# Kernel tuning notes

Measured on AMD Instinct MI355X. Metric: run time of the kernel, lower is better.

## Reference

```python
import jax, jax.numpy as jnp
import numpy as np
import math

B, L, D_MODEL = 2, 2048, 1024
N_HEADS, D_HEAD = 16, 64
ROPE_BASE = 10000.0
PERIODS = (24, 168)
LAMBDAS = (0.5, 0.25)
NEG_INF = jnp.float32(-jnp.inf)


def _alibi_slopes(n_heads):
    # n_heads is a power of two here (16), so only the simple branch is needed
    start = 2.0 ** (-2.0 ** (-(math.log2(n_heads) - 3)))
    return jnp.asarray([start * (start ** i) for i in range(n_heads)], dtype=jnp.float32)


def _apply_rope(x, cos_t, sin_t):
    # x: [B,H,L,Dh]; cos_t/sin_t: [1,1,L,Dh//2]
    x1, x2 = x[..., 0::2], x[..., 1::2]
    xr1 = x1 * cos_t - x2 * sin_t
    xr2 = x1 * sin_t + x2 * cos_t
    return jnp.stack([xr1, xr2], axis=-1).reshape(x.shape)


def setup_inputs() -> dict:
    key = jax.random.key(0)
    ks = jax.random.split(key, 5)
    d = D_MODEL
    return {
        "x": jax.random.normal(ks[0], (B, L, d), dtype=jnp.float32),
        "Wq": jax.random.normal(ks[1], (d, d), dtype=jnp.float32) * 0.02,
        "bq": jnp.zeros((d,), dtype=jnp.float32),
        "Wk": jax.random.normal(ks[2], (d, d), dtype=jnp.float32) * 0.02,
        "bk": jnp.zeros((d,), dtype=jnp.float32),
        "Wv": jax.random.normal(ks[3], (d, d), dtype=jnp.float32) * 0.02,
        "bv": jnp.zeros((d,), dtype=jnp.float32),
        "Wo": jax.random.normal(ks[4], (d, d), dtype=jnp.float32) * 0.02,
        "bo": jnp.zeros((d,), dtype=jnp.float32),
    }


def reference(x, Wq, bq, Wk, bk, Wv, bv, Wo, bo):
    Bn, Ln, Dn = x.shape
    H, Dh = N_HEADS, D_HEAD

    def proj(W, b):
        return (x @ W + b).reshape(Bn, Ln, H, Dh).transpose(0, 2, 1, 3)  # [B,H,L,Dh]

    q, k, v = proj(Wq, bq), proj(Wk, bk), proj(Wv, bv)

    # RoPE angles: theta[l, m] = l / base^(2m/Dh)
    inv = 1.0 / (ROPE_BASE ** (jnp.arange(0, Dh, 2, dtype=jnp.float32) / Dh))
    theta = jnp.arange(Ln, dtype=jnp.float32)[:, None] * inv[None, :]  # [L, Dh/2]
    cos_t = jnp.cos(theta)[None, None]
    sin_t = jnp.sin(theta)[None, None]
    q = _apply_rope(q, cos_t, sin_t)
    k = _apply_rope(k, cos_t, sin_t)

    scale = 1.0 / math.sqrt(Dh)
    attn = jnp.einsum("bhid,bhjd->bhij", q, k) * scale  # [B,H,L,L]

    i = jnp.arange(Ln)[:, None]
    j = jnp.arange(Ln)[None, :]

    # ALiBi bias: -slope * relu(j - i), per head
    slopes = _alibi_slopes(H)  # [H]
    dist = (j - i).astype(jnp.float32)
    attn = attn + (-slopes[None, :, None, None]) * jax.nn.relu(dist)[None, None]

    # periodic cosine bias
    d_abs = jnp.abs(dist)
    pb = jnp.zeros_like(d_abs)
    for P, lam in zip(PERIODS, LAMBDAS):
        pb = pb + lam * jnp.cos(2.0 * math.pi * d_abs / float(P))
    attn = attn + pb[None, None]

    # causal mask (torch: attn + full(-inf).triu(1))
    attn = jnp.where((j > i)[None, None], NEG_INF, attn)

    p = jax.nn.softmax(attn, axis=-1)  # dropout=0 -> identity
    out = jnp.einsum("bhij,bhjd->bhid", p, v)
    out = out.transpose(0, 2, 1, 3).reshape(Bn, Ln, Dn)
    return out @ Wo + bo, p
```

## Files before the change

### kernel.cpp

```cpp
#include <hip/hip_runtime.h>
#include <math.h>

#define B_  2
#define L_  2048
#define D_  1024
#define H_  16
#define DH_ 64
#define BL_ (B_*L_)

typedef unsigned short u16;
typedef __attribute__((ext_vector_type(8))) short short8;
typedef __attribute__((ext_vector_type(4))) float f32x4;
typedef __attribute__((ext_vector_type(4))) unsigned short u16x4;

template<bool V> struct BC { static constexpr bool value = V; };

#define WS_XB   0
#define WS_WT4  2097152
#define WS_QB   4194304
#define WS_KB   6291456
#define WS_VT   8388608
#define WS_AOB  10485760
#define WS_COS  12582912
#define WS_SIN  12648448
#define WS_PBL  12713984

__device__ __forceinline__ u16 f2b(float f) {
  union { float f; unsigned u; } v; v.f = f;
  unsigned r = (v.u + 0x7fffu + ((v.u >> 16) & 1u)) >> 16;
  return (u16)r;
}
__device__ __forceinline__ u16x4 f2b4(float a, float b, float c, float d) {
  u16x4 u; u.x = f2b(a); u.y = f2b(b); u.z = f2b(c); u.w = f2b(d); return u;
}
__device__ __forceinline__ float bf2f(u16 u) {
  union { unsigned u; float f; } v; v.u = ((unsigned)u) << 16; return v.f;
}
__device__ __forceinline__ void gl_lds16(const void* g, void* l) {
  __builtin_amdgcn_global_load_lds(
      (const __attribute__((address_space(1))) unsigned int*)g,
      (__attribute__((address_space(3))) unsigned int*)l, 16, 0, 0);
}
__device__ __forceinline__ void nt_store4(float x, float y, float z, float w, float* p) {
  f32x4 v = (f32x4){x, y, z, w};
  __builtin_nontemporal_store(v, (f32x4*)p);
}

__global__ void fill_tables(float* __restrict__ costab, float* __restrict__ sintab,
                            float* __restrict__ pbl) {
  int idx = blockIdx.x * 256 + threadIdx.x;
  if (idx < L_ * 32) {
    int l = idx >> 5, tp = idx & 31;
    double inv = pow(10000.0, -2.0 * (double)tp / 64.0);
    double th  = (double)l * inv;
    costab[idx] = (float)cos(th);
    sintab[idx] = (float)sin(th);
  }
  if (idx < L_) {
    double d = (double)idx;
    double v = 0.5  * cos(6.283185307179586 * d / 24.0)
             + 0.25 * cos(6.283185307179586 * d / 168.0);
    pbl[idx] = (float)(v * 1.4426950408889634);
  }
}

__global__ __launch_bounds__(256) void xcast(const float* __restrict__ x, u16* __restrict__ xb) {
  const size_t i = ((size_t)blockIdx.x * 256 + threadIdx.x) * 8;
  float4 a = *(const float4*)(x + i);
  float4 b = *(const float4*)(x + i + 4);
  u16 us[8] = { f2b(a.x),f2b(a.y),f2b(a.z),f2b(a.w), f2b(b.x),f2b(b.y),f2b(b.z),f2b(b.w) };
  *(short8*)(xb + i) = *(short8*)us;
}

__global__ __launch_bounds__(256) void wtrans4(const float* __restrict__ W0, const float* __restrict__ W1,
                                               const float* __restrict__ W2, const float* __restrict__ W3,
                                               u16* __restrict__ Wt) {
  __shared__ u16 tt[64][80];
  const int z = blockIdx.z;
  const float* W = (z == 0) ? W0 : (z == 1) ? W1 : (z == 2) ? W2 : W3;
  u16* Wtz = Wt + (size_t)z * 1024 * 1024;
  const int k0 = blockIdx.x << 6, n0 = blockIdx.y << 6;
  const int t = threadIdx.x;
  {
    const int r = t >> 4, c4 = (t & 15) << 2;
    for (int rr = r; rr < 64; rr += 16) {
      float4 v = *(const float4*)(W + (size_t)(k0 + rr) * D_ + n0 + c4);
      tt[c4+0][rr] = f2b(v.x); tt[c4+1][rr] = f2b(v.y);
      tt[c4+2][rr] = f2b(v.z); tt[c4+3][rr] = f2b(v.w);
    }
  }
  __syncthreads();
  const int n = t >> 2, kc = (t & 3) << 4;
  u16* dst = Wtz + (size_t)(n0 + n) * D_ + k0 + kc;
  #pragma unroll
  for (int u = 0; u < 16; ++u) dst[u] = tt[n][kc + u];
}

template<int KIND>
__global__ __launch_bounds__(256) void gemm_k(
    const u16* __restrict__ Ag, const u16* __restrict__ Bg,
    const float* __restrict__ b0, const float* __restrict__ b1, const float* __restrict__ b2,
    const float* __restrict__ costab, const float* __restrict__ sintab,
    u16* __restrict__ O0, u16* __restrict__ O1, u16* __restrict__ O2,
    float* __restrict__ Cout)
{
  __shared__ u16 As[8192];
  __shared__ u16 Bs[8192];
  const int t = threadIdx.x, w = t >> 6, lane = t & 63;
  const int lt = lane & 15, lg = lane >> 4;
  const int row0 = blockIdx.x << 7;
  const int gy   = blockIdx.y;
  const int col0 = gy << 7;
  const int wm = (w & 1) << 6, wn = (w >> 1) << 6;
  const int proj = (KIND == 1) ? (gy >> 3) : 0;
  const bool swp = (KIND == 0) || (proj < 2);

  const int srow = lane >> 3;
  const int gch  = (lane & 7) ^ (srow & 7);
  const u16* aptr[4]; const u16* bptr[4];
  char* adst[4]; char* bdst[4];
  #pragma unroll
  for (int u = 0; u < 4; ++u) {
    const int rl = w * 32 + u * 8 + srow;
    aptr[u] = Ag + (size_t)(row0 + rl) * 1024 + gch * 8;
    bptr[u] = Bg + (size_t)(col0 + rl) * 1024 + gch * 8;
    adst[u] = (char*)As + (w * 32 + u * 8) * 128;
    bdst[u] = (char*)Bs + (w * 32 + u * 8) * 128;
  }
  int aoff[2][4], boff[2][4];
  #pragma unroll
  for (int ks = 0; ks < 2; ++ks)
    #pragma unroll
    for (int q = 0; q < 4; ++q) {
      const int ra = wm + q * 16 + lt;
      aoff[ks][q] = ra * 128 + (((ks * 4 + lg) ^ (ra & 7)) << 4);
      const int rb = wn + q * 16 + lt;
      boff[ks][q] = rb * 128 + (((ks * 4 + lg) ^ (rb & 7)) << 4);
    }

  f32x4 acc[4][4];
  #pragma unroll
  for (int i = 0; i < 4; ++i)
    #pragma unroll
    for (int j = 0; j < 4; ++j) acc[i][j] = (f32x4){0.f,0.f,0.f,0.f};

  auto loop = [&](auto SW) {
    for (int kt = 0; kt < 16; ++kt) {
      #pragma unroll
      for (int u = 0; u < 4; ++u) {
        gl_lds16(aptr[u] + kt * 64, adst[u]);
        gl_lds16(bptr[u] + kt * 64, bdst[u]);
      }
      __syncthreads();
      #pragma unroll
      for (int ks = 0; ks < 2; ++ks) {
        short8 af[4], bf[4];
        #pragma unroll
        for (int q = 0; q < 4; ++q) {
          af[q] = *(const short8*)((const char*)As + aoff[ks][q]);
          bf[q] = *(const short8*)((const char*)Bs + boff[ks][q]);
        }
        #pragma unroll
        for (int mi = 0; mi < 4; ++mi)
          #pragma unroll
          for (int nj = 0; nj < 4; ++nj) {
            if constexpr (decltype(SW)::value)
              acc[mi][nj] = __builtin_amdgcn_mfma_f32_16x16x32_bf16(bf[nj], af[mi], acc[mi][nj], 0, 0, 0);
            else
              acc[mi][nj] = __builtin_amdgcn_mfma_f32_16x16x32_bf16(af[mi], bf[nj], acc[mi][nj], 0, 0, 0);
          }
      }
      __syncthreads();
    }
  };
  if (swp) loop(BC<true>{}); else loop(BC<false>{});

  if constexpr (KIND == 0) {
    #pragma unroll
    for (int mi = 0; mi < 4; ++mi) {
      const int m = row0 + wm + mi * 16 + lt;
      #pragma unroll
      for (int nj = 0; nj < 4; ++nj) {
        const int nb = col0 + wn + nj * 16 + (lg << 2);
        float4 bb = *(const float4*)(b0 + nb);
        nt_store4(acc[mi][nj][0] + bb.x, acc[mi][nj][1] + bb.y,
                  acc[mi][nj][2] + bb.z, acc[mi][nj][3] + bb.w,
                  Cout + (size_t)m * 1024 + nb);
      }
    }
  } else if (proj < 2) {
    const float* bias = proj ? b1 : b0;
    u16* Ob = proj ? O1 : O0;
    const int col0p = (gy & 7) << 7;
    #pragma unroll
    for (int mi = 0; mi < 4; ++mi) {
      const int m = row0 + wm + mi * 16 + lt;
      const int bb_ = m >> 11, lpos = m & (L_ - 1);
      #pragma unroll
      for (int nj = 0; nj < 4; ++nj) {
        const int nb = col0p + wn + nj * 16 + (lg << 2);
        const int d0 = nb & 63, h = nb >> 6;
        float4 ba = *(const float4*)(bias + nb);
        const float o0 = acc[mi][nj][0] + ba.x, o1 = acc[mi][nj][1] + ba.y;
        const float o2 = acc[mi][nj][2] + ba.z, o3 = acc[mi][nj][3] + ba.w;
        const float* ct = costab + lpos * 32 + (d0 >> 1);
        const float* st = sintab + lpos * 32 + (d0 >> 1);
        const float c0 = ct[0], c1 = ct[1], s0 = st[0], s1 = st[1];
        const float r0 = o0 * c0 - o1 * s0, r1 = o0 * s0 + o1 * c0;
        const float r2 = o2 * c1 - o3 * s1, r3 = o2 * s1 + o3 * c1;
        *(u16x4*)(Ob + ((size_t)(bb_ * 16 + h) * L_ + lpos) * 64 + d0) = f2b4(r0, r1, r2, r3);
      }
    }
  } else {
    const int col0p = (gy & 7) << 7;
    #pragma unroll
    for (int mi = 0; mi < 4; ++mi) {
      const int lb = row0 + wm + mi * 16 + (lg << 2);
      const int bb_ = lb >> 11;
      #pragma unroll
      for (int nj = 0; nj < 4; ++nj) {
        const int n = col0p + wn + nj * 16 + lt;
        const int h = n >> 6, dh = n & 63;
        const float bv1 = b2[n];
        *(u16x4*)(O2 + ((size_t)(bb_ * 16 + h) * 64 + dh) * L_ + (lb & (L_ - 1))) =
            f2b4(acc[mi][nj][0] + bv1, acc[mi][nj][1] + bv1,
                 acc[mi][nj][2] + bv1, acc[mi][nj][3] + bv1);
      }
    }
  }
}

__global__ __launch_bounds__(512, 4) void attn_mfma(
    const u16* __restrict__ Qb, const u16* __restrict__ Kb, const u16* __restrict__ Vt,
    const float* __restrict__ pbg, float* __restrict__ Pout, u16* __restrict__ AOb)
{
  __shared__ u16 PL[33 * 16 * 64];
  __shared__ float PVacc[2][16][64];
  __shared__ float lsbuf[8][2][16];
  const int t = threadIdx.x, w = t >> 6, lane = t & 63;
  const int lt = lane & 15, lg = lane >> 4;
  const int wg = blockIdx.x + (blockIdx.y << 6);
  const int sid = (wg & 7) * 256 + (wg >> 3);
  const int bh = sid >> 6, pr = sid & 63;
  const int b = bh >> 4, h = bh & 15;
  const int sA = pr, sB = 127 - pr;
  const int kvA = (sA >> 2) + 1, kvB = (sB >> 2) + 1;
  const int swz = (lt & 7) << 4;
  const float C1 = 0.18033688011112042f;
  char* PLb = (char*)PL;

  f32x4 oaccA[4], oaccB[4];
  #pragma unroll
  for (int dt = 0; dt < 4; ++dt) {
    oaccA[dt] = (f32x4){0.f,0.f,0.f,0.f};
    oaccB[dt] = (f32x4){0.f,0.f,0.f,0.f};
  }
  float lsumA = 0.f, lsumB = 0.f;

  auto tile = [&](int s, int kvt, const short8& q0, const short8& q1,
                  f32x4* oacc, float& lsum, int pb0, int rstride, bool masked) {
    const int j0 = kvt << 6;
    const int i  = s * 16 + lt;
    const u16* kp = Kb + ((size_t)bh * L_ + j0 + lt) * 64 + lg * 8;
    short8 kf[8];
    #pragma unroll
    for (int jt = 0; jt < 4; ++jt) {
      kf[2*jt]   = *(const short8*)(kp + jt * 1024);
      kf[2*jt+1] = *(const short8*)(kp + jt * 1024 + 32);
    }
    f32x4 z[4];
    #pragma unroll
    for (int jt = 0; jt < 4; ++jt) {
      f32x4 zz = (f32x4){0.f,0.f,0.f,0.f};
      zz = __builtin_amdgcn_mfma_f32_16x16x32_bf16(kf[2*jt],   q0, zz, 0, 0, 0);
      zz = __builtin_amdgcn_mfma_f32_16x16x32_bf16(kf[2*jt+1], q1, zz, 0, 0, 0);
      z[jt] = zz;
    }
    const u16* vp = Vt + ((size_t)bh * 64 + lt) * L_ + j0 + lg * 8;
    short8 vf[8];
    #pragma unroll
    for (int dt = 0; dt < 4; ++dt) {
      vf[2*dt]   = *(const short8*)(vp + dt * 16 * L_);
      vf[2*dt+1] = *(const short8*)(vp + dt * 16 * L_ + 32);
    }
    #pragma unroll
    for (int jt = 0; jt < 4; ++jt) {
      const int jb = j0 + jt * 16 + (lg << 2);
      const int dd = i - jb;
      float pr4[4];
      if (masked) {
        #pragma unroll
        for (int r = 0; r < 4; ++r) {
          const int d  = dd - r;
          const int dc = d < 0 ? 0 : d;
          const float pe = exp2f(fmaf(z[jt][r], C1, pbg[dc]));
          pr4[r] = d < 0 ? 0.f : pe;
          lsum += pr4[r];
        }
      } else {
        #pragma unroll
        for (int r = 0; r < 4; ++r) {
          pr4[r] = exp2f(fmaf(z[jt][r], C1, pbg[dd - r]));
          lsum += pr4[r];
        }
      }
      *(u16x4*)(PLb + pb0 + lt * rstride + ((kvt * 128 + jt * 32 + lg * 8) ^ swz)) =
          f2b4(pr4[0], pr4[1], pr4[2], pr4[3]);
    }
    short8 pa0 = *(const short8*)(PLb + pb0 + lt * rstride + ((kvt * 128 + lg * 16) ^ swz));
    short8 pa1 = *(const short8*)(PLb + pb0 + lt * rstride + ((kvt * 128 + 64 + lg * 16) ^ swz));
    #pragma unroll
    for (int dt = 0; dt < 4; ++dt) {
      oacc[dt] = __builtin_amdgcn_mfma_f32_16x16x32_bf16(pa0, vf[2*dt],   oacc[dt], 0, 0, 0);
      oacc[dt] = __builtin_amdgcn_mfma_f32_16x16x32_bf16(pa1, vf[2*dt+1], oacc[dt], 0, 0, 0);
    }
  };

  {
    const u16* qpA = Qb + ((size_t)bh * L_ + sA * 16 + lt) * 64 + lg * 8;
    const short8 qA0 = *(const short8*)(qpA), qA1 = *(const short8*)(qpA + 32);
    for (int kvt = w; kvt < kvA; kvt += 8)
      tile(sA, kvt, qA0, qA1, oaccA, lsumA, 0, kvA << 7, kvt == kvA - 1);
  }
  {
    const u16* qpB = Qb + ((size_t)bh * L_ + sB * 16 + lt) * 64 + lg * 8;
    const short8 qB0 = *(const short8*)(qpB), qB1 = *(const short8*)(qpB + 32);
    const int st0 = (8 + w - (kvA & 7)) & 7;
    for (int kvt = st0; kvt < kvB; kvt += 8)
      tile(sB, kvt, qB0, qB1, oaccB, lsumB, kvA << 11, kvB << 7, kvt == kvB - 1);
  }

  lsumA += __shfl_xor(lsumA, 16); lsumA += __shfl_xor(lsumA, 32);
  lsumB += __shfl_xor(lsumB, 16); lsumB += __shfl_xor(lsumB, 32);
  if (lane < 16) { lsbuf[w][0][lt] = lsumA; lsbuf[w][1][lt] = lsumB; }
  __syncthreads();

  {
    const int rowslot = t >> 4, ct = t & 15;
    const int st = rowslot >> 4, rl = rowslot & 15;
    const int s_ = st ? sB : sA;
    const int i  = s_ * 16 + rl;
    float den = 0.f;
    #pragma unroll
    for (int ww = 0; ww < 8; ++ww) den += lsbuf[ww][st][rl];
    const float rv = 1.f / den;
    const char* rb = PLb + (st ? (kvA << 11) : 0) + rl * ((st ? kvB : kvA) << 7);
    const int rsw = (rl & 7) << 4;
    float* prow = Pout + ((size_t)bh * L_ + i) * L_;
    const int lim4 = i >> 2;
    for (int cc = 0; cc < 8; ++cc) {
      const int c4b = ct + cc * 64;
      u16x4 dv[4];
      #pragma unroll
      for (int u = 0; u < 4; ++u) {
        const int c4 = c4b + u * 16;
        dv[u] = (c4 <= lim4) ? *(const u16x4*)(rb + ((c4 << 3) ^ rsw))
                             : (u16x4){0, 0, 0, 0};
      }
      #pragma unroll
      for (int u = 0; u < 4; ++u) {
        const int c4 = c4b + u * 16;
        float ox = 0.f, oy = 0.f, oz = 0.f, ow = 0.f;
        if (c4 <= lim4) {
          ox = bf2f(dv[u].x) * rv; oy = bf2f(dv[u].y) * rv;
          oz = bf2f(dv[u].z) * rv; ow = bf2f(dv[u].w) * rv;
          if (c4 == lim4) {
            const int j0c = c4 << 2;
            if (j0c + 1 > i) oy = 0.f;
            if (j0c + 2 > i) oz = 0.f;
            if (j0c + 3 > i) ow = 0.f;
          }
        }
        nt_store4(ox, oy, oz, ow, prow + (c4 << 2));
      }
    }
  }

  for (int rr = 0; rr < 8; ++rr) {
    if (w == rr) {
      #pragma unroll
      for (int dt = 0; dt < 4; ++dt)
        #pragma unroll
        for (int r = 0; r < 4; ++r) {
          if (rr == 0) {
            PVacc[0][(lg << 2) + r][dt * 16 + lt] = oaccA[dt][r];
            PVacc[1][(lg << 2) + r][dt * 16 + lt] = oaccB[dt][r];
          } else {
            PVacc[0][(lg << 2) + r][dt * 16 + lt] += oaccA[dt][r];
            PVacc[1][(lg << 2) + r][dt * 16 + lt] += oaccB[dt][r];
          }
        }
    }
    __syncthreads();
  }

  {
    const int st = t >> 8, rl = (t >> 4) & 15, c0 = (t & 15) << 2;
    float den = 0.f;
    #pragma unroll
    for (int ww = 0; ww < 8; ++ww) den += lsbuf[ww][st][rl];
    const float rv = 1.f / den;
    const int s_ = st ? sB : sA;
    const int i = s_ * 16 + rl;
    u16x4 o = f2b4(PVacc[st][rl][c0] * rv, PVacc[st][rl][c0 + 1] * rv,
                   PVacc[st][rl][c0 + 2] * rv, PVacc[st][rl][c0 + 3] * rv);
    *(u16x4*)(AOb + ((size_t)(b * L_ + i)) * 1024 + h * 64 + c0) = o;
  }
}

extern "C" void kernel_launch(void* const* d_in, const int* in_sizes, int n_in,
                              void* d_out, int out_size, void* d_ws, size_t ws_size,
                              hipStream_t stream) {
  const float* x  = (const float*)d_in[0];
  const float* Wq = (const float*)d_in[1];
  const float* bq = (const float*)d_in[2];
  const float* Wk = (const float*)d_in[3];
  const float* bk = (const float*)d_in[4];
  const float* Wv = (const float*)d_in[5];
  const float* bv = (const float*)d_in[6];
  const float* Wo = (const float*)d_in[7];
  const float* bo = (const float*)d_in[8];

  float* out  = (float*)d_out;
  float* Pout = out + (size_t)BL_ * D_;

  float* ws = (float*)d_ws;
  u16* XB  = (u16*)(ws + WS_XB);
  u16* WT4 = (u16*)(ws + WS_WT4);
  u16* QB  = (u16*)(ws + WS_QB);
  u16* KB  = (u16*)(ws + WS_KB);
  u16* VT  = (u16*)(ws + WS_VT);
  u16* AOB = (u16*)(ws + WS_AOB);
  float* cosT = ws + WS_COS;
  float* sinT = ws + WS_SIN;
  float* pblG = ws + WS_PBL;

  fill_tables<<<256, 256, 0, stream>>>(cosT, sinT, pblG);
  xcast<<<2048, 256, 0, stream>>>(x, XB);
  wtrans4<<<dim3(16,16,4), 256, 0, stream>>>(Wq, Wk, Wv, Wo, WT4);

  gemm_k<1><<<dim3(32,24), 256, 0, stream>>>(XB, WT4, bq, bk, bv, cosT, sinT,
                                             QB, KB, VT, nullptr);

  attn_mfma<<<dim3(64,32), 512, 0, stream>>>(QB, KB, VT, pblG, Pout, AOB);

  gemm_k<0><<<dim3(32,8), 256, 0, stream>>>(AOB, WT4 + (size_t)3*1024*1024, bo,
                                            nullptr, nullptr, nullptr, nullptr,
                                            nullptr, nullptr, nullptr, out);
}
```

Baseline: 285.9 us.

## Stage periodic bias in LDS, remap GEMM blocks, store P rows per wavefront

Three separate changes. The GEMM kernels remap block indices so that consecutive workgroups are spread across XCD-strided groups, aiming for better L2 locality. The attention kernel copies the periodic-bias table into the PVacc shared buffer before the main loop, so the per-element bias lookups read LDS instead of global memory; this costs an extra barrier and reuses PVacc. The probability writeback now gives each wavefront whole rows, so every store instruction covers a contiguous 1 KB span of a row rather than several rows.

```diff
diff --git a/kernel.cpp b/kernel.cpp
--- a/kernel.cpp
+++ b/kernel.cpp
@@ -108,8 +108,12 @@
   __shared__ u16 Bs[8192];
   const int t = threadIdx.x, w = t >> 6, lane = t & 63;
   const int lt = lane & 15, lg = lane >> 4;
-  const int row0 = blockIdx.x << 7;
-  const int gy   = blockIdx.y;
+  const int wg = blockIdx.x + (blockIdx.y << 5);
+  int sid;
+  if constexpr (KIND == 1) sid = (wg & 7) * 96 + (wg >> 3);
+  else                     sid = (wg & 7) * 32 + (wg >> 3);
+  const int row0 = (sid & 31) << 7;
+  const int gy   = sid >> 5;
   const int col0 = gy << 7;
   const int wm = (w & 1) << 6, wn = (w >> 1) << 6;
   const int proj = (KIND == 1) ? (gy >> 3) : 0;
@@ -237,8 +241,10 @@
   __shared__ u16 PL[33 * 16 * 64];
   __shared__ float PVacc[2][16][64];
   __shared__ float lsbuf[8][2][16];
+  float* pbl = &PVacc[0][0][0];
   const int t = threadIdx.x, w = t >> 6, lane = t & 63;
   const int lt = lane & 15, lg = lane >> 4;
+  *(float4*)(pbl + t * 4) = *(const float4*)(pbg + t * 4);
   const int wg = blockIdx.x + (blockIdx.y << 6);
   const int sid = (wg & 7) * 256 + (wg >> 3);
   const int bh = sid >> 6, pr = sid & 63;
@@ -248,6 +254,7 @@
   const int swz = (lt & 7) << 4;
   const float C1 = 0.18033688011112042f;
   char* PLb = (char*)PL;
+  __syncthreads();
 
   f32x4 oaccA[4], oaccB[4];
   #pragma unroll
@@ -293,14 +300,14 @@
         for (int r = 0; r < 4; ++r) {
           const int d  = dd - r;
           const int dc = d < 0 ? 0 : d;
-          const float pe = exp2f(fmaf(z[jt][r], C1, pbg[dc]));
+          const float pe = exp2f(fmaf(z[jt][r], C1, pbl[dc]));
           pr4[r] = d < 0 ? 0.f : pe;
           lsum += pr4[r];
         }
       } else {
         #pragma unroll
         for (int r = 0; r < 4; ++r) {
-          pr4[r] = exp2f(fmaf(z[jt][r], C1, pbg[dd - r]));
+          pr4[r] = exp2f(fmaf(z[jt][r], C1, pbl[dd - r]));
           lsum += pr4[r];
         }
       }
@@ -335,9 +342,10 @@
   if (lane < 16) { lsbuf[w][0][lt] = lsumA; lsbuf[w][1][lt] = lsumB; }
   __syncthreads();
 
-  {
-    const int rowslot = t >> 4, ct = t & 15;
-    const int st = rowslot >> 4, rl = rowslot & 15;
+  #pragma unroll
+  for (int rp = 0; rp < 4; ++rp) {
+    const int rid = rp * 8 + w;
+    const int st = rid >> 4, rl = rid & 15;
     const int s_ = st ? sB : sA;
     const int i  = s_ * 16 + rl;
     float den = 0.f;
@@ -348,31 +356,22 @@
     const int rsw = (rl & 7) << 4;
     float* prow = Pout + ((size_t)bh * L_ + i) * L_;
     const int lim4 = i >> 2;
+    #pragma unroll
     for (int cc = 0; cc < 8; ++cc) {
-      const int c4b = ct + cc * 64;
-      u16x4 dv[4];
-      #pragma unroll
-      for (int u = 0; u < 4; ++u) {
-        const int c4 = c4b + u * 16;
-        dv[u] = (c4 <= lim4) ? *(const u16x4*)(rb + ((c4 << 3) ^ rsw))
-                             : (u16x4){0, 0, 0, 0};
-      }
-      #pragma unroll
-      for (int u = 0; u < 4; ++u) {
-        const int c4 = c4b + u * 16;
-        float ox = 0.f, oy = 0.f, oz = 0.f, ow = 0.f;
-        if (c4 <= lim4) {
-          ox = bf2f(dv[u].x) * rv; oy = bf2f(dv[u].y) * rv;
-          oz = bf2f(dv[u].z) * rv; ow = bf2f(dv[u].w) * rv;
-          if (c4 == lim4) {
-            const int j0c = c4 << 2;
-            if (j0c + 1 > i) oy = 0.f;
-            if (j0c + 2 > i) oz = 0.f;
-            if (j0c + 3 > i) ow = 0.f;
-          }
+      const int c4 = lane + cc * 64;
+      float ox = 0.f, oy = 0.f, oz = 0.f, ow = 0.f;
+      if (c4 <= lim4) {
+        u16x4 dv = *(const u16x4*)(rb + ((c4 << 3) ^ rsw));
+        ox = bf2f(dv.x) * rv; oy = bf2f(dv.y) * rv;
+        oz = bf2f(dv.z) * rv; ow = bf2f(dv.w) * rv;
+        if (c4 == lim4) {
+          const int j0c = c4 << 2;
+          if (j0c + 1 > i) oy = 0.f;
+          if (j0c + 2 > i) oz = 0.f;
+          if (j0c + 3 > i) ow = 0.f;
         }
-        nt_store4(ox, oy, oz, ow, prow + (c4 << 2));
-      }
+      }
+      nt_store4(ox, oy, oz, ow, prow + (c4 << 2));
     }
   }
 
```

Measured after the change: 256.9 us. 10.1% less time.
